# Performance work log

Measured on AMD Instinct MI355X. Metric: run time of the kernel, lower is better.

The kernel has to match this reference:

```python
import jax, jax.numpy as jnp
import numpy as np

B, N, D = 8, 1024, 768
H = 12
HD = D // H
LN_EPS = 1e-5
EPS = 1e-8


def setup_inputs() -> dict:
    key = jax.random.key(0)
    ks = jax.random.split(key, 16)
    s = 0.02
    return {
        "x": jax.random.normal(ks[0], (B, N, D), jnp.float32),
        "low_freq_feat": jax.random.normal(ks[1], (B, N, D), jnp.float32),
        "high_freq_feat": jax.random.normal(ks[2], (B, N, D), jnp.float32),
        "W_qkv_id": jax.random.normal(ks[3], (D, 3 * D), jnp.float32) * s,
        "W_qkv_attr": jax.random.normal(ks[4], (D, 3 * D), jnp.float32) * s,
        "W_fg_id": jax.random.normal(ks[5], (D, D), jnp.float32) * s,
        "b_fg_id": jnp.zeros((D,), jnp.float32),
        "W_fg_attr": jax.random.normal(ks[6], (D, D), jnp.float32) * s,
        "b_fg_attr": jnp.zeros((D,), jnp.float32),
        "W_proj_id": jax.random.normal(ks[7], (D, D), jnp.float32) * s,
        "b_proj_id": jnp.zeros((D,), jnp.float32),
        "W_proj_attr": jax.random.normal(ks[8], (D, D), jnp.float32) * s,
        "b_proj_attr": jnp.zeros((D,), jnp.float32),
        "ln_id_g": jnp.ones((D,), jnp.float32),
        "ln_id_b": jnp.zeros((D,), jnp.float32),
        "ln_attr_g": jnp.ones((D,), jnp.float32),
        "ln_attr_b": jnp.zeros((D,), jnp.float32),
        "ortho_temperature": jnp.float32(1.0),
        "freq_guide_strength": jnp.float32(0.3),
    }


def _layernorm(x, g, b):
    mu = x.mean(-1, keepdims=True)
    var = ((x - mu) ** 2).mean(-1, keepdims=True)
    return (x - mu) * jax.lax.rsqrt(var + LN_EPS) * g + b


def reference(x, low_freq_feat, high_freq_feat,
              W_qkv_id, W_qkv_attr,
              W_fg_id, b_fg_id, W_fg_attr, b_fg_attr,
              W_proj_id, b_proj_id, W_proj_attr, b_proj_attr,
              ln_id_g, ln_id_b, ln_attr_g, ln_attr_b,
              ortho_temperature, freq_guide_strength):
    b, n, d = x.shape
    scale = HD ** -0.5

    def split_qkv(t):
        t = t.reshape(b, n, 3, H, HD).transpose(2, 0, 3, 1, 4)
        return t[0], t[1], t[2]

    q_id, k_id, v_id = split_qkv(x @ W_qkv_id)
    q_at, k_at, v_at = split_qkv(x @ W_qkv_attr)

    fs = jax.nn.sigmoid(freq_guide_strength)
    low_g = (low_freq_feat @ W_fg_id + b_fg_id).reshape(b, n, H, HD).transpose(0, 2, 1, 3)
    high_g = (high_freq_feat @ W_fg_attr + b_fg_attr).reshape(b, n, H, HD).transpose(0, 2, 1, 3)
    v_id = v_id + fs * low_g
    v_at = v_at + fs * high_g

    def soft_attn(q, k):
        a = jnp.clip(jnp.einsum('bhnd,bhmd->bhnm', q, k) * scale, -20.0, 20.0)
        return jax.nn.softmax(a, axis=-1)

    attn_id = soft_attn(q_id, k_id)
    attn_at = soft_attn(q_at, k_at)

    # soft orthogonal mask (same mask for both branches)
    overlap = ((attn_id + EPS) * (attn_at + EPS)).sum(-1, keepdims=True)
    temp = jnp.clip(ortho_temperature, 0.1, 5.0)
    mask = jax.nn.sigmoid(-overlap * temp)

    def mask_renorm(a):
        m = a * mask
        m = m / (m.sum(-1, keepdims=True) + EPS)
        return jnp.where(jnp.isnan(m), jnp.zeros_like(m), m)

    attn_id = mask_renorm(attn_id)
    attn_at = mask_renorm(attn_at)

    def branch_out(a, v, W, bias, g, beta):
        o = jnp.einsum('bhnm,bhmd->bhnd', a, v).transpose(0, 2, 1, 3).reshape(b, n, d)
        return _layernorm(o @ W + bias, g, beta)

    id_features = branch_out(attn_id, v_id, W_proj_id, b_proj_id, ln_id_g, ln_id_b)
    attr_features = branch_out(attn_at, v_at, W_proj_attr, b_proj_attr, ln_attr_g, ln_attr_b)
    return (id_features, attr_features)
```

## Files before the change

kernel.cpp:

```cpp
#include <hip/hip_runtime.h>
#include <stdint.h>


typedef __attribute__((ext_vector_type(8))) _Float16 f16x8;
typedef __attribute__((ext_vector_type(4))) _Float16 f16x4;
typedef __attribute__((ext_vector_type(4))) float    f32x4;

__device__ __forceinline__ void g2l16(const void* g, void* l) {
  __builtin_amdgcn_global_load_lds(
      (const __attribute__((address_space(1))) void*)g,
      (__attribute__((address_space(3))) void*)l, 16, 0, 0);
}

template <bool SWAP>
__device__ __forceinline__ void gemm128(const _Float16* __restrict__ A,
                                        const _Float16* __restrict__ Bt,
                                        int K, int m0, int n0,
                                        _Float16* As, _Float16* Bs, f32x4* acc) {
  const int tid = threadIdx.x;
  const int lane = tid & 63, w = tid >> 6;
  const int wm = (w >> 1) * 64, wn = (w & 1) * 64;
  const int l15 = lane & 15, quad = lane >> 4;
  const int srow = lane >> 2;
  const int scol = ((lane & 3) ^ ((lane >> 3) & 3)) * 8;
  const int rg = (quad ^ ((l15 >> 1) & 3)) * 8;

#pragma unroll
  for (int i = 0; i < 16; i++) acc[i] = (f32x4){0.f, 0.f, 0.f, 0.f};

  const int KB = K >> 6;
#pragma unroll
  for (int k2 = 0; k2 < 2; k2++)
#pragma unroll
    for (int i = 0; i < 2; i++) {
      int c = w * 2 + i, row = c * 16 + srow;
      g2l16(A  + (size_t)(m0 + row) * K + k2 * 32 + scol, As + k2 * 4096 + c * 512);
      g2l16(Bt + (size_t)(n0 + row) * K + k2 * 32 + scol, Bs + k2 * 4096 + c * 512);
    }
  for (int kb = 0; kb < KB; kb++) {
    __syncthreads();
#pragma unroll
    for (int k2 = 0; k2 < 2; k2++) {
      f16x8 a[4], b[4];
#pragma unroll
      for (int mt = 0; mt < 4; mt++)
        a[mt] = *(const f16x8*)(As + k2 * 4096 + (wm + mt * 16 + l15) * 32 + rg);
#pragma unroll
      for (int nt = 0; nt < 4; nt++)
        b[nt] = *(const f16x8*)(Bs + k2 * 4096 + (wn + nt * 16 + l15) * 32 + rg);
#pragma unroll
      for (int mt = 0; mt < 4; mt++)
#pragma unroll
        for (int nt = 0; nt < 4; nt++)
          acc[mt * 4 + nt] = SWAP
              ? __builtin_amdgcn_mfma_f32_16x16x32_f16(b[nt], a[mt], acc[mt * 4 + nt], 0, 0, 0)
              : __builtin_amdgcn_mfma_f32_16x16x32_f16(a[mt], b[nt], acc[mt * 4 + nt], 0, 0, 0);
    }
    __syncthreads();
    if (kb + 1 < KB) {
      int k0 = (kb + 1) * 64;
#pragma unroll
      for (int k2 = 0; k2 < 2; k2++)
#pragma unroll
        for (int i = 0; i < 2; i++) {
          int c = w * 2 + i, row = c * 16 + srow;
          g2l16(A  + (size_t)(m0 + row) * K + k0 + k2 * 32 + scol, As + k2 * 4096 + c * 512);
          g2l16(Bt + (size_t)(n0 + row) * K + k0 + k2 * 32 + scol, Bs + k2 * 4096 + c * 512);
        }
    }
  }
}

__global__ __launch_bounds__(256) void k_cast3(const float* __restrict__ s0,
                                               const float* __restrict__ s1,
                                               const float* __restrict__ s2,
                                               _Float16* __restrict__ d0,
                                               _Float16* __restrict__ d1,
                                               _Float16* __restrict__ d2) {
  int blk = blockIdx.x;
  const float* s; _Float16* d;
  if (blk < 6144)       { s = s0; d = d0; }
  else if (blk < 12288) { s = s1; d = d1; blk -= 6144; }
  else                  { s = s2; d = d2; blk -= 12288; }
  int i = blk * 256 + threadIdx.x;
  float4 v = ((const float4*)s)[i];
  f16x4 o = {(_Float16)v.x, (_Float16)v.y, (_Float16)v.z, (_Float16)v.w};
  *(f16x4*)(d + (size_t)i * 4) = o;
}

__device__ __forceinline__ void tcast32(const float* __restrict__ src,
                                        _Float16* __restrict__ dst,
                                        int N, int n0, int k0) {
  __shared__ float t[32][33];
  int tr = threadIdx.x >> 5, tc = threadIdx.x & 31;
#pragma unroll
  for (int i = 0; i < 4; i++) {
    int r = tr + i * 8;
    t[r][tc] = src[(size_t)(k0 + r) * N + n0 + tc];
  }
  __syncthreads();
#pragma unroll
  for (int i = 0; i < 4; i++) {
    int r = tr + i * 8;
    dst[(size_t)(n0 + r) * 768 + k0 + tc] = (_Float16)t[tc][r];
  }
}

__global__ __launch_bounds__(256) void k_tcast_all(const float* __restrict__ Wq0,
                                                   const float* __restrict__ Wq1,
                                                   const float* __restrict__ W0,
                                                   const float* __restrict__ W1,
                                                   const float* __restrict__ W2,
                                                   const float* __restrict__ W3,
                                                   _Float16* __restrict__ Dq,
                                                   _Float16* __restrict__ D0,
                                                   _Float16* __restrict__ D1,
                                                   _Float16* __restrict__ D2,
                                                   _Float16* __restrict__ D3) {
  int blk = blockIdx.x;
  if (blk < 3456) {
    int half = blk / 1728, rem = blk % 1728;
    int xx = rem % 72, yy = rem / 72;
    tcast32(half ? Wq1 : Wq0, Dq + (size_t)half * 2304 * 768, 2304, xx * 32, yy * 32);
  } else {
    blk -= 3456;
    int q = blk / 576, rem = blk % 576;
    int xx = rem % 24, yy = rem / 24;
    const float* src; _Float16* d;
    if (q == 0)      { src = W0; d = D0; }
    else if (q == 1) { src = W1; d = D1; }
    else if (q == 2) { src = W2; d = D2; }
    else             { src = W3; d = D3; }
    tcast32(src, d, 768, xx * 32, yy * 32);
  }
}

__global__ __launch_bounds__(256) void k_gemm_qkv(const _Float16* __restrict__ A,
                                                  const _Float16* __restrict__ Bt,
                                                  _Float16* __restrict__ Qb,
                                                  _Float16* __restrict__ Kb,
                                                  _Float16* __restrict__ Vtb) {
  __shared__ alignas(16) _Float16 As[8192], Bs[8192];
  f32x4 acc[16];
  int m0 = blockIdx.y * 128, n0 = blockIdx.x * 128;
  int br = n0 / 2304;
  int three = (n0 - br * 2304) / 768;
  int lane = threadIdx.x & 63, w = threadIdx.x >> 6;
  int wm = (w >> 1) * 64, wn = (w & 1) * 64, l15 = lane & 15, quad = lane >> 4;

  if (three == 2) {
    gemm128<false>(A, Bt, 768, m0, n0, As, Bs, acc);
#pragma unroll
    for (int mt = 0; mt < 4; mt++)
#pragma unroll
      for (int nt = 0; nt < 4; nt++) {
        int n = n0 + wn + nt * 16 + l15;
        int c = n - br * 2304 - 1536;
        int h = c >> 6, hd = c & 63;
        int m = m0 + wm + mt * 16 + quad * 4;
        int b = m >> 10, tok = m & 1023;
        size_t head = (size_t)(br * 96 + b * 12 + h);
        f32x4 v = acc[mt * 4 + nt];
        f16x4 o;
#pragma unroll
        for (int r = 0; r < 4; r++) o[r] = (_Float16)v[r];
        *(f16x4*)(Vtb + (head * 64 + hd) * 1024 + tok) = o;
      }
  } else {
    gemm128<true>(A, Bt, 768, m0, n0, As, Bs, acc);
    float qscl = (three == 0) ? 0.125f * 1.44269504f : 1.0f;
    _Float16* dst = (three == 0) ? Qb : Kb;
#pragma unroll
    for (int mt = 0; mt < 4; mt++)
#pragma unroll
      for (int nt = 0; nt < 4; nt++) {
        int m = m0 + wm + mt * 16 + l15;
        int n = n0 + wn + nt * 16 + quad * 4;
        int c = n - br * 2304 - three * 768;
        int h = c >> 6, hd = c & 63;
        int b = m >> 10, tok = m & 1023;
        size_t head = (size_t)(br * 96 + b * 12 + h);
        f32x4 v = acc[mt * 4 + nt];
        f16x4 o;
#pragma unroll
        for (int r = 0; r < 4; r++) o[r] = (_Float16)(v[r] * qscl);
        *(f16x4*)(dst + (head * 1024 + tok) * 64 + hd) = o;
      }
  }
}

__global__ __launch_bounds__(256) void k_gemm_fgadd(const _Float16* __restrict__ Alo,
                                                    const _Float16* __restrict__ Ahi,
                                                    const _Float16* __restrict__ Bid,
                                                    const _Float16* __restrict__ Bat,
                                                    const float* __restrict__ bid,
                                                    const float* __restrict__ bat,
                                                    const float* __restrict__ fgs,
                                                    _Float16* __restrict__ Vtb) {
  __shared__ alignas(16) _Float16 As[8192], Bs[8192];
  f32x4 acc[16];
  int br = blockIdx.x / 6;
  int n0 = (blockIdx.x % 6) * 128, m0 = blockIdx.y * 128;
  const _Float16* A = br ? Ahi : Alo;
  const _Float16* Bt = br ? Bat : Bid;
  const float* bias = br ? bat : bid;
  gemm128<false>(A, Bt, 768, m0, n0, As, Bs, acc);
  float fs = 1.f / (1.f + __expf(-fgs[0]));
  int lane = threadIdx.x & 63, w = threadIdx.x >> 6;
  int wm = (w >> 1) * 64, wn = (w & 1) * 64, l15 = lane & 15, quad = lane >> 4;
#pragma unroll
  for (int mt = 0; mt < 4; mt++)
#pragma unroll
    for (int nt = 0; nt < 4; nt++) {
      int c = n0 + wn + nt * 16 + l15;
      int h = c >> 6, hd = c & 63;
      int m = m0 + wm + mt * 16 + quad * 4;
      int b = m >> 10, tok = m & 1023;
      size_t head = (size_t)(br * 96 + b * 12 + h);
      float bv = bias[c];
      f32x4 v = acc[mt * 4 + nt];
      _Float16* p = Vtb + (head * 64 + hd) * 1024 + tok;
      f16x4 old = *(const f16x4*)p;
      f16x4 o;
#pragma unroll
      for (int r = 0; r < 4; r++)
        o[r] = (_Float16)((float)old[r] + fs * (v[r] + bv));
      *(f16x4*)p = o;
    }
}

__global__ __launch_bounds__(256, 3) void k_attn(const _Float16* __restrict__ Qb,
                                                 const _Float16* __restrict__ Kb,
                                                 const _Float16* __restrict__ Vtb,
                                                 _Float16* __restrict__ Ob) {
  __shared__ alignas(16) _Float16 Qs[128 * 64];
  __shared__ alignas(16) _Float16 Ks[128 * 64];
  __shared__ alignas(16) _Float16 Vts[64 * 128];
  int hl = blockIdx.x;
  int br = hl / 96, bh = hl % 96;
  int qbase = blockIdx.y * 128;
  const _Float16* Qh = Qb + (size_t)hl * 65536;
  const _Float16* Kh = Kb + (size_t)hl * 65536;
  const _Float16* Vth = Vtb + (size_t)hl * 65536;
  int lane = threadIdx.x & 63, w = threadIdx.x >> 6;
  int l15 = lane & 15, quad = lane >> 4;
  const int key7 = l15 & 7;

  {
    int rr = lane >> 3, sg = (lane & 7) ^ rr;
#pragma unroll
    for (int i = 0; i < 4; i++) {
      int c = w * 4 + i;
      g2l16(Qh + (size_t)(qbase + c * 8 + rr) * 64 + sg * 8, Qs + c * 512);
    }
  }
  auto stage_kv = [&](int n0) {
    int rr8 = lane >> 3, sg8 = ((lane & 7) ^ rr8) * 8;
    int rr16 = lane >> 4;
#pragma unroll
    for (int i = 0; i < 4; i++) {
      int c = w * 4 + i;
      g2l16(Kh + (size_t)(n0 + c * 8 + rr8) * 64 + sg8, Ks + c * 512);
      int vrow = c * 4 + rr16;
      int sg16 = ((lane & 15) ^ (vrow & 15)) * 8;
      g2l16(Vth + (size_t)vrow * 1024 + n0 + sg16, Vts + c * 512);
    }
  };
  stage_kv(0);

  f32x4 o[2][4];
#pragma unroll
  for (int qg = 0; qg < 2; qg++)
#pragma unroll
    for (int i = 0; i < 4; i++) o[qg][i] = (f32x4){0.f, 0.f, 0.f, 0.f};
  float rs0 = 0.f, rs1 = 0.f;
  f16x8 bq[2][2];
  const f32x4 zero = (f32x4){0.f, 0.f, 0.f, 0.f};
  const int g0 = (quad ^ key7) * 8, g1 = ((4 + quad) ^ key7) * 8;

  for (int kt = 0; kt < 8; kt++) {
    __syncthreads();
    if (kt == 0) {
#pragma unroll
      for (int qg = 0; qg < 2; qg++) {
        bq[qg][0] = *(const f16x8*)(Qs + (w * 32 + qg * 16 + l15) * 64 + g0);
        bq[qg][1] = *(const f16x8*)(Qs + (w * 32 + qg * 16 + l15) * 64 + g1);
      }
    }
    f32x4 c0, c1;
    {
      f16x8 a0 = *(const f16x8*)(Ks + l15 * 64 + g0);
      f16x8 a1 = *(const f16x8*)(Ks + l15 * 64 + g1);
      c0 = __builtin_amdgcn_mfma_f32_16x16x32_f16(a0, bq[0][0], zero, 0, 0, 0);
      c0 = __builtin_amdgcn_mfma_f32_16x16x32_f16(a1, bq[0][1], c0, 0, 0, 0);
      c1 = __builtin_amdgcn_mfma_f32_16x16x32_f16(a0, bq[1][0], zero, 0, 0, 0);
      c1 = __builtin_amdgcn_mfma_f32_16x16x32_f16(a1, bq[1][1], c1, 0, 0, 0);
    }
#pragma unroll
    for (int nt = 0; nt < 8; nt++) {
      f32x4 n0_, n1_;
      if (nt < 7) {
        f16x8 a0 = *(const f16x8*)(Ks + ((nt + 1) * 16 + l15) * 64 + g0);
        f16x8 a1 = *(const f16x8*)(Ks + ((nt + 1) * 16 + l15) * 64 + g1);
        n0_ = __builtin_amdgcn_mfma_f32_16x16x32_f16(a0, bq[0][0], zero, 0, 0, 0);
        n0_ = __builtin_amdgcn_mfma_f32_16x16x32_f16(a1, bq[0][1], n0_, 0, 0, 0);
        n1_ = __builtin_amdgcn_mfma_f32_16x16x32_f16(a0, bq[1][0], zero, 0, 0, 0);
        n1_ = __builtin_amdgcn_mfma_f32_16x16x32_f16(a1, bq[1][1], n1_, 0, 0, 0);
      }
      f16x4 pt0, pt1;
#pragma unroll
      for (int r = 0; r < 4; r++) {
        float p = __builtin_amdgcn_exp2f(c0[r]);
        rs0 += p; pt0[r] = (_Float16)p;
      }
#pragma unroll
      for (int r = 0; r < 4; r++) {
        float p = __builtin_amdgcn_exp2f(c1[r]);
        rs1 += p; pt1[r] = (_Float16)p;
      }
#pragma unroll
      for (int hdt = 0; hdt < 4; hdt++) {
        int g = ((2 * nt + (quad >> 1)) ^ l15) * 8 + (quad & 1) * 4;
        f16x4 av = *(const f16x4*)(Vts + (hdt * 16 + l15) * 128 + g);
        o[0][hdt] = __builtin_amdgcn_mfma_f32_16x16x16f16(av, pt0, o[0][hdt], 0, 0, 0);
        o[1][hdt] = __builtin_amdgcn_mfma_f32_16x16x16f16(av, pt1, o[1][hdt], 0, 0, 0);
      }
      if (nt < 7) { c0 = n0_; c1 = n1_; }
    }
    __syncthreads();
    if (kt < 7) stage_kv((kt + 1) * 128);
  }
  int b = bh / 12, h = bh % 12;
#pragma unroll
  for (int qg = 0; qg < 2; qg++) {
    float l = qg ? rs1 : rs0;
    l += __shfl_xor(l, 16);
    l += __shfl_xor(l, 32);
    float inv = 1.f / l;
    size_t rowb = ((size_t)br * 8192 + b * 1024 + qbase + w * 32 + qg * 16 + l15) * 768 +
                  h * 64;
#pragma unroll
    for (int hdt = 0; hdt < 4; hdt++) {
      f16x4 u;
#pragma unroll
      for (int r = 0; r < 4; r++) u[r] = (_Float16)(o[qg][hdt][r] * inv);
      *(f16x4*)(Ob + rowb + hdt * 16 + quad * 4) = u;
    }
  }
}

__global__ __launch_bounds__(256) void k_gemm_proj2(const _Float16* __restrict__ Aid,
                                                    const _Float16* __restrict__ Aat,
                                                    const _Float16* __restrict__ Bid,
                                                    const _Float16* __restrict__ Bat,
                                                    _Float16* __restrict__ Yid,
                                                    _Float16* __restrict__ Yat) {
  __shared__ alignas(16) _Float16 As[8192], Bs[8192];
  f32x4 acc[16];
  int half = blockIdx.x / 6;
  int n0 = (blockIdx.x % 6) * 128, m0 = blockIdx.y * 128;
  const _Float16* A = half ? Aat : Aid;
  const _Float16* Bt = half ? Bat : Bid;
  _Float16* Y = half ? Yat : Yid;
  gemm128<true>(A, Bt, 768, m0, n0, As, Bs, acc);
  int lane = threadIdx.x & 63, w = threadIdx.x >> 6;
  int wm = (w >> 1) * 64, wn = (w & 1) * 64, l15 = lane & 15, quad = lane >> 4;
#pragma unroll
  for (int mt = 0; mt < 4; mt++)
#pragma unroll
    for (int nt = 0; nt < 4; nt++) {
      int m = m0 + wm + mt * 16 + l15;
      int n = n0 + wn + nt * 16 + quad * 4;
      f32x4 v = acc[mt * 4 + nt];
      f16x4 o;
#pragma unroll
      for (int r = 0; r < 4; r++) o[r] = (_Float16)v[r];
      *(f16x4*)(Y + (size_t)m * 768 + n) = o;
    }
}

__global__ __launch_bounds__(256) void k_ln(const _Float16* __restrict__ Yid,
                                            const _Float16* __restrict__ Yat,
                                            const float* __restrict__ bp_id,
                                            const float* __restrict__ bp_at,
                                            const float* __restrict__ g_id,
                                            const float* __restrict__ be_id,
                                            const float* __restrict__ g_at,
                                            const float* __restrict__ be_at,
                                            float* __restrict__ out) {
  int w = threadIdx.x >> 6, lane = threadIdx.x & 63;
  int r = blockIdx.x * 4 + w;
  int br = r >> 13, m = r & 8191;
  const _Float16* Y = br ? Yat : Yid;
  const float* bp = br ? bp_at : bp_id;
  const float* g = br ? g_at : g_id;
  const float* be = br ? be_at : be_id;
  float v[12], sum = 0.f, sq = 0.f;
#pragma unroll
  for (int j = 0; j < 3; j++) {
    int c = j * 256 + lane * 4;
    f16x4 y = *(const f16x4*)(Y + (size_t)m * 768 + c);
    float4 bv = *(const float4*)(bp + c);
#pragma unroll
    for (int r2 = 0; r2 < 4; r2++) {
      float t = (float)y[r2] + ((const float*)&bv)[r2];
      v[j * 4 + r2] = t; sum += t; sq += t * t;
    }
  }
#pragma unroll
  for (int d = 1; d < 64; d <<= 1) { sum += __shfl_xor(sum, d); sq += __shfl_xor(sq, d); }
  float mu = sum * (1.f / 768.f);
  float var = sq * (1.f / 768.f) - mu * mu;
  float rstd = rsqrtf(var + 1e-5f);
  float* op = out + (size_t)br * 6291456 + (size_t)m * 768;
#pragma unroll
  for (int j = 0; j < 3; j++) {
    int c = j * 256 + lane * 4;
    float4 gv = *(const float4*)(g + c);
    float4 bev = *(const float4*)(be + c);
    float4 ov;
#pragma unroll
    for (int r2 = 0; r2 < 4; r2++)
      ((float*)&ov)[r2] = (v[j * 4 + r2] - mu) * rstd * ((const float*)&gv)[r2] +
                          ((const float*)&bev)[r2];
    *(float4*)(op + c) = ov;
  }
}

extern "C" void kernel_launch(void* const* d_in, const int* in_sizes, int n_in,
                              void* d_out, int out_size, void* d_ws, size_t ws_size,
                              hipStream_t stream) {
  const float* x       = (const float*)d_in[0];
  const float* lowf    = (const float*)d_in[1];
  const float* highf   = (const float*)d_in[2];
  const float* Wqkv_id = (const float*)d_in[3];
  const float* Wqkv_at = (const float*)d_in[4];
  const float* Wfg_id  = (const float*)d_in[5];
  const float* bfg_id  = (const float*)d_in[6];
  const float* Wfg_at  = (const float*)d_in[7];
  const float* bfg_at  = (const float*)d_in[8];
  const float* Wpr_id  = (const float*)d_in[9];
  const float* bpr_id  = (const float*)d_in[10];
  const float* Wpr_at  = (const float*)d_in[11];
  const float* bpr_at  = (const float*)d_in[12];
  const float* g_id    = (const float*)d_in[13];
  const float* be_id   = (const float*)d_in[14];
  const float* g_at    = (const float*)d_in[15];
  const float* be_at   = (const float*)d_in[16];
  const float* fgs     = (const float*)d_in[18];

  char* ws = (char*)d_ws;
  _Float16* x_f    = (_Float16*)(ws + 0);
  _Float16* low_f  = (_Float16*)(ws + 12582912);
  _Float16* high_f = (_Float16*)(ws + 25165824);
  _Float16* wqkvt  = (_Float16*)(ws + 37748736);
  _Float16* wfgidt = (_Float16*)(ws + 44826624);
  _Float16* wfgatt = (_Float16*)(ws + 46006272);
  _Float16* wpridt = (_Float16*)(ws + 47185920);
  _Float16* wpratt = (_Float16*)(ws + 48365568);
  _Float16* Qb     = (_Float16*)(ws + 74711040);
  _Float16* Kb     = (_Float16*)(ws + 99876864);
  _Float16* Vtb    = (_Float16*)(ws + 125042688);
  _Float16* Ob     = (_Float16*)(ws + 150208512);
  _Float16* Y_id   = (_Float16*)(ws + 0);
  _Float16* Y_at   = (_Float16*)(ws + 49545216);

  k_cast3<<<18432, 256, 0, stream>>>(x, lowf, highf, x_f, low_f, high_f);
  k_tcast_all<<<5760, 256, 0, stream>>>(Wqkv_id, Wqkv_at, Wfg_id, Wfg_at, Wpr_id, Wpr_at,
                                        wqkvt, wfgidt, wfgatt, wpridt, wpratt);
  k_gemm_qkv<<<dim3(36, 64), 256, 0, stream>>>(x_f, wqkvt, Qb, Kb, Vtb);
  k_gemm_fgadd<<<dim3(12, 64), 256, 0, stream>>>(low_f, high_f, wfgidt, wfgatt,
                                                 bfg_id, bfg_at, fgs, Vtb);
  k_attn<<<dim3(192, 8), 256, 0, stream>>>(Qb, Kb, Vtb, Ob);
  k_gemm_proj2<<<dim3(12, 64), 256, 0, stream>>>(Ob, Ob + 6291456, wpridt, wpratt,
                                                 Y_id, Y_at);
  k_ln<<<4096, 256, 0, stream>>>(Y_id, Y_at, bpr_id, bpr_at, g_id, be_id, g_at, be_at,
                                 (float*)d_out);
}
```

Measured before the change: 423.0 us.

## Switch GEMMs to 256x256 tiles with 4-stage async LDS ring pipeline

Replaces the 128x128, 256-thread, double-sync GEMM core with a 256x256 tile computed by 512 threads (8 waves, each owning 128x64). It uses a 4-deep LDS ring buffer filled by global_load_lds, with explicit vmcnt waits and raw s_barriers, and splits A and B stage loads across two half-tiles. It also raises MFMA issue priority with s_setprio. The aim is more operand reuse per loaded byte and overlapping global-to-LDS transfers with MFMA work. The trade-off is 128KB of LDS per block, so likely one block per CU, and the fg and proj GEMMs now launch only 192 blocks, which risks underfilling the GPU and longer tails.

```diff
diff --git a/kernel.cpp b/kernel.cpp
--- a/kernel.cpp
+++ b/kernel.cpp
@@ -12,63 +12,102 @@
       (__attribute__((address_space(3))) void*)l, 16, 0, 0);
 }
 
+#define BARX()   asm volatile("s_barrier" ::: "memory")
+#define WAITV(N) asm volatile("s_waitcnt vmcnt(" #N ")" ::: "memory")
+
 template <bool SWAP>
-__device__ __forceinline__ void gemm128(const _Float16* __restrict__ A,
+__device__ __forceinline__ void gemm256(const _Float16* __restrict__ A,
                                         const _Float16* __restrict__ Bt,
                                         int K, int m0, int n0,
-                                        _Float16* As, _Float16* Bs, f32x4* acc) {
+                                        _Float16* As, _Float16* Bs,
+                                        f32x4 (&acc)[8][4]) {
   const int tid = threadIdx.x;
   const int lane = tid & 63, w = tid >> 6;
-  const int wm = (w >> 1) * 64, wn = (w & 1) * 64;
+  const int wm = (w >> 2) * 128, wn = (w & 3) * 64;
   const int l15 = lane & 15, quad = lane >> 4;
   const int srow = lane >> 2;
   const int scol = ((lane & 3) ^ ((lane >> 3) & 3)) * 8;
   const int rg = (quad ^ ((l15 >> 1) & 3)) * 8;
-
-#pragma unroll
-  for (int i = 0; i < 16; i++) acc[i] = (f32x4){0.f, 0.f, 0.f, 0.f};
-
-  const int KB = K >> 6;
-#pragma unroll
-  for (int k2 = 0; k2 < 2; k2++)
-#pragma unroll
-    for (int i = 0; i < 2; i++) {
-      int c = w * 2 + i, row = c * 16 + srow;
-      g2l16(A  + (size_t)(m0 + row) * K + k2 * 32 + scol, As + k2 * 4096 + c * 512);
-      g2l16(Bt + (size_t)(n0 + row) * K + k2 * 32 + scol, Bs + k2 * 4096 + c * 512);
-    }
-  for (int kb = 0; kb < KB; kb++) {
-    __syncthreads();
-#pragma unroll
-    for (int k2 = 0; k2 < 2; k2++) {
-      f16x8 a[4], b[4];
-#pragma unroll
-      for (int mt = 0; mt < 4; mt++)
-        a[mt] = *(const f16x8*)(As + k2 * 4096 + (wm + mt * 16 + l15) * 32 + rg);
-#pragma unroll
-      for (int nt = 0; nt < 4; nt++)
-        b[nt] = *(const f16x8*)(Bs + k2 * 4096 + (wn + nt * 16 + l15) * 32 + rg);
-#pragma unroll
-      for (int mt = 0; mt < 4; mt++)
-#pragma unroll
-        for (int nt = 0; nt < 4; nt++)
-          acc[mt * 4 + nt] = SWAP
-              ? __builtin_amdgcn_mfma_f32_16x16x32_f16(b[nt], a[mt], acc[mt * 4 + nt], 0, 0, 0)
-              : __builtin_amdgcn_mfma_f32_16x16x32_f16(a[mt], b[nt], acc[mt * 4 + nt], 0, 0, 0);
-    }
-    __syncthreads();
-    if (kb + 1 < KB) {
-      int k0 = (kb + 1) * 64;
-#pragma unroll
-      for (int k2 = 0; k2 < 2; k2++)
-#pragma unroll
-        for (int i = 0; i < 2; i++) {
-          int c = w * 2 + i, row = c * 16 + srow;
-          g2l16(A  + (size_t)(m0 + row) * K + k0 + k2 * 32 + scol, As + k2 * 4096 + c * 512);
-          g2l16(Bt + (size_t)(n0 + row) * K + k0 + k2 * 32 + scol, Bs + k2 * 4096 + c * 512);
-        }
-    }
-  }
+  const int c0 = w * 2, c1 = c0 + 1;
+  const _Float16* pA0 = A + (m0 + c0 * 16 + srow) * K + scol;
+  const _Float16* pA1 = A + (m0 + c1 * 16 + srow) * K + scol;
+  const _Float16* pB0 = Bt + (n0 + c0 * 16 + srow) * K + scol;
+  const _Float16* pB1 = Bt + (n0 + c1 * 16 + srow) * K + scol;
+
+#pragma unroll
+  for (int mt = 0; mt < 8; mt++)
+#pragma unroll
+    for (int nt = 0; nt < 4; nt++) acc[mt][nt] = (f32x4){0.f, 0.f, 0.f, 0.f};
+
+  const int KT = K >> 5;
+
+#pragma unroll
+  for (int t = 0; t < 3; t++) {
+    int kc = t * 32, bj = t * 8192;
+    g2l16(pA0 + kc, As + bj + c0 * 512);
+    g2l16(pB0 + kc, Bs + bj + c0 * 512);
+    g2l16(pA1 + kc, As + bj + c1 * 512);
+    g2l16(pB1 + kc, Bs + bj + c1 * 512);
+  }
+  WAITV(8);
+  BARX();
+
+  auto tile = [&](int t, bool doStage) {
+    const int bj = (t & 3) * 8192;
+    const _Float16* as = As + bj;
+    const _Float16* bs = Bs + bj;
+    const int kcn = (t + 3) * 32;
+    const int bn = ((t + 3) & 3) * 8192;
+    f16x8 a[8];
+#pragma unroll
+    for (int mt = 0; mt < 8; mt++)
+      a[mt] = *(const f16x8*)(as + (wm + mt * 16 + l15) * 32 + rg);
+    f16x8 b0 = *(const f16x8*)(bs + (wn + l15) * 32 + rg);
+    f16x8 b1 = *(const f16x8*)(bs + (wn + 16 + l15) * 32 + rg);
+    if (doStage) {
+      g2l16(pA0 + kcn, As + bn + c0 * 512);
+      g2l16(pA1 + kcn, As + bn + c1 * 512);
+    }
+    __builtin_amdgcn_s_setprio(1);
+#pragma unroll
+    for (int mt = 0; mt < 8; mt++) {
+      acc[mt][0] = SWAP
+          ? __builtin_amdgcn_mfma_f32_16x16x32_f16(b0, a[mt], acc[mt][0], 0, 0, 0)
+          : __builtin_amdgcn_mfma_f32_16x16x32_f16(a[mt], b0, acc[mt][0], 0, 0, 0);
+      acc[mt][1] = SWAP
+          ? __builtin_amdgcn_mfma_f32_16x16x32_f16(b1, a[mt], acc[mt][1], 0, 0, 0)
+          : __builtin_amdgcn_mfma_f32_16x16x32_f16(a[mt], b1, acc[mt][1], 0, 0, 0);
+    }
+    __builtin_amdgcn_s_setprio(0);
+    BARX();
+    f16x8 b2 = *(const f16x8*)(bs + (wn + 32 + l15) * 32 + rg);
+    f16x8 b3 = *(const f16x8*)(bs + (wn + 48 + l15) * 32 + rg);
+    if (doStage) {
+      g2l16(pB0 + kcn, Bs + bn + c0 * 512);
+      g2l16(pB1 + kcn, Bs + bn + c1 * 512);
+    }
+    __builtin_amdgcn_s_setprio(1);
+#pragma unroll
+    for (int mt = 0; mt < 8; mt++) {
+      acc[mt][2] = SWAP
+          ? __builtin_amdgcn_mfma_f32_16x16x32_f16(b2, a[mt], acc[mt][2], 0, 0, 0)
+          : __builtin_amdgcn_mfma_f32_16x16x32_f16(a[mt], b2, acc[mt][2], 0, 0, 0);
+      acc[mt][3] = SWAP
+          ? __builtin_amdgcn_mfma_f32_16x16x32_f16(b3, a[mt], acc[mt][3], 0, 0, 0)
+          : __builtin_amdgcn_mfma_f32_16x16x32_f16(a[mt], b3, acc[mt][3], 0, 0, 0);
+    }
+    __builtin_amdgcn_s_setprio(0);
+  };
+
+  int t = 0;
+  for (; t < KT - 3; ++t) {
+    tile(t, true);
+    WAITV(8);
+    BARX();
+  }
+  tile(t, false); WAITV(4); BARX(); ++t;
+  tile(t, false); WAITV(0); BARX(); ++t;
+  tile(t, false);
 }
 
 __global__ __launch_bounds__(256) void k_cast3(const float* __restrict__ s0,
@@ -135,23 +174,23 @@
   }
 }
 
-__global__ __launch_bounds__(256) void k_gemm_qkv(const _Float16* __restrict__ A,
-                                                  const _Float16* __restrict__ Bt,
-                                                  _Float16* __restrict__ Qb,
-                                                  _Float16* __restrict__ Kb,
-                                                  _Float16* __restrict__ Vtb) {
-  __shared__ alignas(16) _Float16 As[8192], Bs[8192];
-  f32x4 acc[16];
-  int m0 = blockIdx.y * 128, n0 = blockIdx.x * 128;
+__global__ __launch_bounds__(512, 2) void k_gemm_qkv(const _Float16* __restrict__ A,
+                                                     const _Float16* __restrict__ Bt,
+                                                     _Float16* __restrict__ Qb,
+                                                     _Float16* __restrict__ Kb,
+                                                     _Float16* __restrict__ Vtb) {
+  __shared__ alignas(16) _Float16 As[32768], Bs[32768];
+  f32x4 acc[8][4];
+  int m0 = blockIdx.y * 256, n0 = blockIdx.x * 256;
   int br = n0 / 2304;
   int three = (n0 - br * 2304) / 768;
   int lane = threadIdx.x & 63, w = threadIdx.x >> 6;
-  int wm = (w >> 1) * 64, wn = (w & 1) * 64, l15 = lane & 15, quad = lane >> 4;
+  int wm = (w >> 2) * 128, wn = (w & 3) * 64, l15 = lane & 15, quad = lane >> 4;
 
   if (three == 2) {
-    gemm128<false>(A, Bt, 768, m0, n0, As, Bs, acc);
-#pragma unroll
-    for (int mt = 0; mt < 4; mt++)
+    gemm256<false>(A, Bt, 768, m0, n0, As, Bs, acc);
+#pragma unroll
+    for (int mt = 0; mt < 8; mt++)
 #pragma unroll
       for (int nt = 0; nt < 4; nt++) {
         int n = n0 + wn + nt * 16 + l15;
@@ -160,18 +199,18 @@
         int m = m0 + wm + mt * 16 + quad * 4;
         int b = m >> 10, tok = m & 1023;
         size_t head = (size_t)(br * 96 + b * 12 + h);
-        f32x4 v = acc[mt * 4 + nt];
+        f32x4 v = acc[mt][nt];
         f16x4 o;
 #pragma unroll
         for (int r = 0; r < 4; r++) o[r] = (_Float16)v[r];
         *(f16x4*)(Vtb + (head * 64 + hd) * 1024 + tok) = o;
       }
   } else {
-    gemm128<true>(A, Bt, 768, m0, n0, As, Bs, acc);
+    gemm256<true>(A, Bt, 768, m0, n0, As, Bs, acc);
     float qscl = (three == 0) ? 0.125f * 1.44269504f : 1.0f;
     _Float16* dst = (three == 0) ? Qb : Kb;
 #pragma unroll
-    for (int mt = 0; mt < 4; mt++)
+    for (int mt = 0; mt < 8; mt++)
 #pragma unroll
       for (int nt = 0; nt < 4; nt++) {
         int m = m0 + wm + mt * 16 + l15;
@@ -180,7 +219,7 @@
         int h = c >> 6, hd = c & 63;
         int b = m >> 10, tok = m & 1023;
         size_t head = (size_t)(br * 96 + b * 12 + h);
-        f32x4 v = acc[mt * 4 + nt];
+        f32x4 v = acc[mt][nt];
         f16x4 o;
 #pragma unroll
         for (int r = 0; r < 4; r++) o[r] = (_Float16)(v[r] * qscl);
@@ -189,27 +228,27 @@
   }
 }
 
-__global__ __launch_bounds__(256) void k_gemm_fgadd(const _Float16* __restrict__ Alo,
-                                                    const _Float16* __restrict__ Ahi,
-                                                    const _Float16* __restrict__ Bid,
-                                                    const _Float16* __restrict__ Bat,
-                                                    const float* __restrict__ bid,
-                                                    const float* __restrict__ bat,
-                                                    const float* __restrict__ fgs,
-                                                    _Float16* __restrict__ Vtb) {
-  __shared__ alignas(16) _Float16 As[8192], Bs[8192];
-  f32x4 acc[16];
-  int br = blockIdx.x / 6;
-  int n0 = (blockIdx.x % 6) * 128, m0 = blockIdx.y * 128;
+__global__ __launch_bounds__(512, 2) void k_gemm_fgadd(const _Float16* __restrict__ Alo,
+                                                       const _Float16* __restrict__ Ahi,
+                                                       const _Float16* __restrict__ Bid,
+                                                       const _Float16* __restrict__ Bat,
+                                                       const float* __restrict__ bid,
+                                                       const float* __restrict__ bat,
+                                                       const float* __restrict__ fgs,
+                                                       _Float16* __restrict__ Vtb) {
+  __shared__ alignas(16) _Float16 As[32768], Bs[32768];
+  f32x4 acc[8][4];
+  int br = blockIdx.x / 3;
+  int n0 = (blockIdx.x % 3) * 256, m0 = blockIdx.y * 256;
   const _Float16* A = br ? Ahi : Alo;
   const _Float16* Bt = br ? Bat : Bid;
   const float* bias = br ? bat : bid;
-  gemm128<false>(A, Bt, 768, m0, n0, As, Bs, acc);
+  gemm256<false>(A, Bt, 768, m0, n0, As, Bs, acc);
   float fs = 1.f / (1.f + __expf(-fgs[0]));
   int lane = threadIdx.x & 63, w = threadIdx.x >> 6;
-  int wm = (w >> 1) * 64, wn = (w & 1) * 64, l15 = lane & 15, quad = lane >> 4;
-#pragma unroll
-  for (int mt = 0; mt < 4; mt++)
+  int wm = (w >> 2) * 128, wn = (w & 3) * 64, l15 = lane & 15, quad = lane >> 4;
+#pragma unroll
+  for (int mt = 0; mt < 8; mt++)
 #pragma unroll
     for (int nt = 0; nt < 4; nt++) {
       int c = n0 + wn + nt * 16 + l15;
@@ -218,7 +257,7 @@
       int b = m >> 10, tok = m & 1023;
       size_t head = (size_t)(br * 96 + b * 12 + h);
       float bv = bias[c];
-      f32x4 v = acc[mt * 4 + nt];
+      f32x4 v = acc[mt][nt];
       _Float16* p = Vtb + (head * 64 + hd) * 1024 + tok;
       f16x4 old = *(const f16x4*)p;
       f16x4 o;
@@ -349,29 +388,29 @@
   }
 }
 
-__global__ __launch_bounds__(256) void k_gemm_proj2(const _Float16* __restrict__ Aid,
-                                                    const _Float16* __restrict__ Aat,
-                                                    const _Float16* __restrict__ Bid,
-                                                    const _Float16* __restrict__ Bat,
-                                                    _Float16* __restrict__ Yid,
-                                                    _Float16* __restrict__ Yat) {
-  __shared__ alignas(16) _Float16 As[8192], Bs[8192];
-  f32x4 acc[16];
-  int half = blockIdx.x / 6;
-  int n0 = (blockIdx.x % 6) * 128, m0 = blockIdx.y * 128;
+__global__ __launch_bounds__(512, 2) void k_gemm_proj2(const _Float16* __restrict__ Aid,
+                                                       const _Float16* __restrict__ Aat,
+                                                       const _Float16* __restrict__ Bid,
+                                                       const _Float16* __restrict__ Bat,
+                                                       _Float16* __restrict__ Yid,
+                                                       _Float16* __restrict__ Yat) {
+  __shared__ alignas(16) _Float16 As[32768], Bs[32768];
+  f32x4 acc[8][4];
+  int half = blockIdx.x / 3;
+  int n0 = (blockIdx.x % 3) * 256, m0 = blockIdx.y * 256;
   const _Float16* A = half ? Aat : Aid;
   const _Float16* Bt = half ? Bat : Bid;
   _Float16* Y = half ? Yat : Yid;
-  gemm128<true>(A, Bt, 768, m0, n0, As, Bs, acc);
+  gemm256<true>(A, Bt, 768, m0, n0, As, Bs, acc);
   int lane = threadIdx.x & 63, w = threadIdx.x >> 6;
-  int wm = (w >> 1) * 64, wn = (w & 1) * 64, l15 = lane & 15, quad = lane >> 4;
-#pragma unroll
-  for (int mt = 0; mt < 4; mt++)
+  int wm = (w >> 2) * 128, wn = (w & 3) * 64, l15 = lane & 15, quad = lane >> 4;
+#pragma unroll
+  for (int mt = 0; mt < 8; mt++)
 #pragma unroll
     for (int nt = 0; nt < 4; nt++) {
       int m = m0 + wm + mt * 16 + l15;
       int n = n0 + wn + nt * 16 + quad * 4;
-      f32x4 v = acc[mt * 4 + nt];
+      f32x4 v = acc[mt][nt];
       f16x4 o;
 #pragma unroll
       for (int r = 0; r < 4; r++) o[r] = (_Float16)v[r];
@@ -468,12 +507,12 @@
   k_cast3<<<18432, 256, 0, stream>>>(x, lowf, highf, x_f, low_f, high_f);
   k_tcast_all<<<5760, 256, 0, stream>>>(Wqkv_id, Wqkv_at, Wfg_id, Wfg_at, Wpr_id, Wpr_at,
                                         wqkvt, wfgidt, wfgatt, wpridt, wpratt);
-  k_gemm_qkv<<<dim3(36, 64), 256, 0, stream>>>(x_f, wqkvt, Qb, Kb, Vtb);
-  k_gemm_fgadd<<<dim3(12, 64), 256, 0, stream>>>(low_f, high_f, wfgidt, wfgatt,
-                                                 bfg_id, bfg_at, fgs, Vtb);
+  k_gemm_qkv<<<dim3(18, 32), 512, 0, stream>>>(x_f, wqkvt, Qb, Kb, Vtb);
+  k_gemm_fgadd<<<dim3(6, 32), 512, 0, stream>>>(low_f, high_f, wfgidt, wfgatt,
+                                                bfg_id, bfg_at, fgs, Vtb);
   k_attn<<<dim3(192, 8), 256, 0, stream>>>(Qb, Kb, Vtb, Ob);
-  k_gemm_proj2<<<dim3(12, 64), 256, 0, stream>>>(Ob, Ob + 6291456, wpridt, wpratt,
-                                                 Y_id, Y_at);
+  k_gemm_proj2<<<dim3(6, 32), 512, 0, stream>>>(Ob, Ob + 6291456, wpridt, wpratt,
+                                                Y_id, Y_at);
   k_ln<<<4096, 256, 0, stream>>>(Y_id, Y_at, bpr_id, bpr_at, g_id, be_id, g_at, be_at,
                                  (float*)d_out);
 }
```

New measurement: 410.3 us. -3.0%, faster.

## Enlarge GEMM tiles to 256x192 with double-buffered LDS and MFMA priority

Applied to the files above, without the earlier changes.

The shared GEMM helper now uses 256x192 block tiles with 512 threads, each wave computing 64x96. LDS is double-buffered so the next K-tile's global-to-LDS loads are issued before the current tile's MFMAs, replacing two __syncthreads per iteration with one vmcnt wait and barrier. The MFMA section also raises wave priority and is fenced with scheduling barriers. The goal is more operand reuse per LDS load, fewer barriers and load latency hidden behind compute. In exchange it uses more LDS and more registers per block, and launches far fewer blocks, which may leave CUs unevenly loaded.

```diff
diff --git a/kernel.cpp b/kernel.cpp
--- a/kernel.cpp
+++ b/kernel.cpp
@@ -12,62 +12,81 @@
       (__attribute__((address_space(3))) void*)l, 16, 0, 0);
 }
 
+#define BARX()   asm volatile("s_barrier" ::: "memory")
+#define WAITV0() asm volatile("s_waitcnt vmcnt(0)" ::: "memory")
+
 template <bool SWAP>
-__device__ __forceinline__ void gemm128(const _Float16* __restrict__ A,
+__device__ __forceinline__ void gemm192(const _Float16* __restrict__ A,
                                         const _Float16* __restrict__ Bt,
                                         int K, int m0, int n0,
-                                        _Float16* As, _Float16* Bs, f32x4* acc) {
+                                        _Float16* As, _Float16* Bs,
+                                        f32x4 (&acc)[4][6]) {
   const int tid = threadIdx.x;
   const int lane = tid & 63, w = tid >> 6;
-  const int wm = (w >> 1) * 64, wn = (w & 1) * 64;
+  const int wm = (w >> 1) * 64, wn = (w & 1) * 96;
   const int l15 = lane & 15, quad = lane >> 4;
   const int srow = lane >> 2;
   const int scol = ((lane & 3) ^ ((lane >> 3) & 3)) * 8;
   const int rg = (quad ^ ((l15 >> 1) & 3)) * 8;
-
-#pragma unroll
-  for (int i = 0; i < 16; i++) acc[i] = (f32x4){0.f, 0.f, 0.f, 0.f};
-
-  const int KB = K >> 6;
-#pragma unroll
-  for (int k2 = 0; k2 < 2; k2++)
-#pragma unroll
-    for (int i = 0; i < 2; i++) {
-      int c = w * 2 + i, row = c * 16 + srow;
-      g2l16(A  + (size_t)(m0 + row) * K + k2 * 32 + scol, As + k2 * 4096 + c * 512);
-      g2l16(Bt + (size_t)(n0 + row) * K + k2 * 32 + scol, Bs + k2 * 4096 + c * 512);
-    }
-  for (int kb = 0; kb < KB; kb++) {
-    __syncthreads();
-#pragma unroll
-    for (int k2 = 0; k2 < 2; k2++) {
-      f16x8 a[4], b[4];
+  const int KT = K >> 6;
+
+  auto stage = [&](int t) {
+    const int kc = t * 64;
+    _Float16* Ab = As + (t & 1) * 16384;
+    _Float16* Bb = Bs + (t & 1) * 12288;
+#pragma unroll
+    for (int h = 0; h < 2; h++)
+#pragma unroll
+      for (int i = 0; i < 2; i++) {
+        int c = w * 2 + i;
+        g2l16(A + (size_t)(m0 + c * 16 + srow) * K + kc + h * 32 + scol,
+              Ab + h * 8192 + c * 512);
+      }
+#pragma unroll
+    for (int i = 0; i < 3; i++) {
+      int j = w * 3 + i;
+      int hb = j / 12, cb = j % 12;
+      g2l16(Bt + (size_t)(n0 + cb * 16 + srow) * K + kc + hb * 32 + scol,
+            Bb + hb * 6144 + cb * 512);
+    }
+  };
+
+#pragma unroll
+  for (int mt = 0; mt < 4; mt++)
+#pragma unroll
+    for (int nt = 0; nt < 6; nt++) acc[mt][nt] = (f32x4){0.f, 0.f, 0.f, 0.f};
+
+  stage(0);
+  WAITV0();
+  BARX();
+
+  for (int t = 0; t < KT; t++) {
+    const _Float16* as = As + (t & 1) * 16384;
+    const _Float16* bs = Bs + (t & 1) * 12288;
+    if (t + 1 < KT) stage(t + 1);
+#pragma unroll
+    for (int ks = 0; ks < 2; ks++) {
+      f16x8 a[4], b[6];
 #pragma unroll
       for (int mt = 0; mt < 4; mt++)
-        a[mt] = *(const f16x8*)(As + k2 * 4096 + (wm + mt * 16 + l15) * 32 + rg);
-#pragma unroll
-      for (int nt = 0; nt < 4; nt++)
-        b[nt] = *(const f16x8*)(Bs + k2 * 4096 + (wn + nt * 16 + l15) * 32 + rg);
+        a[mt] = *(const f16x8*)(as + ks * 8192 + (wm + mt * 16 + l15) * 32 + rg);
+#pragma unroll
+      for (int nt = 0; nt < 6; nt++)
+        b[nt] = *(const f16x8*)(bs + ks * 6144 + (wn + nt * 16 + l15) * 32 + rg);
+      __builtin_amdgcn_sched_barrier(0);
+      __builtin_amdgcn_s_setprio(1);
 #pragma unroll
       for (int mt = 0; mt < 4; mt++)
 #pragma unroll
-        for (int nt = 0; nt < 4; nt++)
-          acc[mt * 4 + nt] = SWAP
-              ? __builtin_amdgcn_mfma_f32_16x16x32_f16(b[nt], a[mt], acc[mt * 4 + nt], 0, 0, 0)
-              : __builtin_amdgcn_mfma_f32_16x16x32_f16(a[mt], b[nt], acc[mt * 4 + nt], 0, 0, 0);
-    }
-    __syncthreads();
-    if (kb + 1 < KB) {
-      int k0 = (kb + 1) * 64;
-#pragma unroll
-      for (int k2 = 0; k2 < 2; k2++)
-#pragma unroll
-        for (int i = 0; i < 2; i++) {
-          int c = w * 2 + i, row = c * 16 + srow;
-          g2l16(A  + (size_t)(m0 + row) * K + k0 + k2 * 32 + scol, As + k2 * 4096 + c * 512);
-          g2l16(Bt + (size_t)(n0 + row) * K + k0 + k2 * 32 + scol, Bs + k2 * 4096 + c * 512);
-        }
-    }
+        for (int nt = 0; nt < 6; nt++)
+          acc[mt][nt] = SWAP
+              ? __builtin_amdgcn_mfma_f32_16x16x32_f16(b[nt], a[mt], acc[mt][nt], 0, 0, 0)
+              : __builtin_amdgcn_mfma_f32_16x16x32_f16(a[mt], b[nt], acc[mt][nt], 0, 0, 0);
+      __builtin_amdgcn_s_setprio(0);
+      __builtin_amdgcn_sched_barrier(0);
+    }
+    WAITV0();
+    BARX();
   }
 }
 
@@ -135,52 +154,52 @@
   }
 }
 
-__global__ __launch_bounds__(256) void k_gemm_qkv(const _Float16* __restrict__ A,
-                                                  const _Float16* __restrict__ Bt,
-                                                  _Float16* __restrict__ Qb,
-                                                  _Float16* __restrict__ Kb,
-                                                  _Float16* __restrict__ Vtb) {
-  __shared__ alignas(16) _Float16 As[8192], Bs[8192];
-  f32x4 acc[16];
-  int m0 = blockIdx.y * 128, n0 = blockIdx.x * 128;
+__global__ __launch_bounds__(512, 2) void k_gemm_qkv(const _Float16* __restrict__ A,
+                                                     const _Float16* __restrict__ Bt,
+                                                     _Float16* __restrict__ Qb,
+                                                     _Float16* __restrict__ Kb,
+                                                     _Float16* __restrict__ Vtb) {
+  __shared__ alignas(16) _Float16 As[32768], Bs[24576];
+  f32x4 acc[4][6];
+  int m0 = blockIdx.y * 256, n0 = blockIdx.x * 192;
   int br = n0 / 2304;
   int three = (n0 - br * 2304) / 768;
   int lane = threadIdx.x & 63, w = threadIdx.x >> 6;
-  int wm = (w >> 1) * 64, wn = (w & 1) * 64, l15 = lane & 15, quad = lane >> 4;
+  int wm = (w >> 1) * 64, wn = (w & 1) * 96, l15 = lane & 15, quad = lane >> 4;
 
   if (three == 2) {
-    gemm128<false>(A, Bt, 768, m0, n0, As, Bs, acc);
+    gemm192<false>(A, Bt, 768, m0, n0, As, Bs, acc);
 #pragma unroll
     for (int mt = 0; mt < 4; mt++)
 #pragma unroll
-      for (int nt = 0; nt < 4; nt++) {
+      for (int nt = 0; nt < 6; nt++) {
         int n = n0 + wn + nt * 16 + l15;
         int c = n - br * 2304 - 1536;
         int h = c >> 6, hd = c & 63;
         int m = m0 + wm + mt * 16 + quad * 4;
         int b = m >> 10, tok = m & 1023;
         size_t head = (size_t)(br * 96 + b * 12 + h);
-        f32x4 v = acc[mt * 4 + nt];
+        f32x4 v = acc[mt][nt];
         f16x4 o;
 #pragma unroll
         for (int r = 0; r < 4; r++) o[r] = (_Float16)v[r];
         *(f16x4*)(Vtb + (head * 64 + hd) * 1024 + tok) = o;
       }
   } else {
-    gemm128<true>(A, Bt, 768, m0, n0, As, Bs, acc);
+    gemm192<true>(A, Bt, 768, m0, n0, As, Bs, acc);
     float qscl = (three == 0) ? 0.125f * 1.44269504f : 1.0f;
     _Float16* dst = (three == 0) ? Qb : Kb;
 #pragma unroll
     for (int mt = 0; mt < 4; mt++)
 #pragma unroll
-      for (int nt = 0; nt < 4; nt++) {
+      for (int nt = 0; nt < 6; nt++) {
         int m = m0 + wm + mt * 16 + l15;
         int n = n0 + wn + nt * 16 + quad * 4;
         int c = n - br * 2304 - three * 768;
         int h = c >> 6, hd = c & 63;
         int b = m >> 10, tok = m & 1023;
         size_t head = (size_t)(br * 96 + b * 12 + h);
-        f32x4 v = acc[mt * 4 + nt];
+        f32x4 v = acc[mt][nt];
         f16x4 o;
 #pragma unroll
         for (int r = 0; r < 4; r++) o[r] = (_Float16)(v[r] * qscl);
@@ -189,36 +208,36 @@
   }
 }
 
-__global__ __launch_bounds__(256) void k_gemm_fgadd(const _Float16* __restrict__ Alo,
-                                                    const _Float16* __restrict__ Ahi,
-                                                    const _Float16* __restrict__ Bid,
-                                                    const _Float16* __restrict__ Bat,
-                                                    const float* __restrict__ bid,
-                                                    const float* __restrict__ bat,
-                                                    const float* __restrict__ fgs,
-                                                    _Float16* __restrict__ Vtb) {
-  __shared__ alignas(16) _Float16 As[8192], Bs[8192];
-  f32x4 acc[16];
-  int br = blockIdx.x / 6;
-  int n0 = (blockIdx.x % 6) * 128, m0 = blockIdx.y * 128;
+__global__ __launch_bounds__(512, 2) void k_gemm_fgadd(const _Float16* __restrict__ Alo,
+                                                       const _Float16* __restrict__ Ahi,
+                                                       const _Float16* __restrict__ Bid,
+                                                       const _Float16* __restrict__ Bat,
+                                                       const float* __restrict__ bid,
+                                                       const float* __restrict__ bat,
+                                                       const float* __restrict__ fgs,
+                                                       _Float16* __restrict__ Vtb) {
+  __shared__ alignas(16) _Float16 As[32768], Bs[24576];
+  f32x4 acc[4][6];
+  int br = blockIdx.x >> 2;
+  int n0 = (blockIdx.x & 3) * 192, m0 = blockIdx.y * 256;
   const _Float16* A = br ? Ahi : Alo;
   const _Float16* Bt = br ? Bat : Bid;
   const float* bias = br ? bat : bid;
-  gemm128<false>(A, Bt, 768, m0, n0, As, Bs, acc);
+  gemm192<false>(A, Bt, 768, m0, n0, As, Bs, acc);
   float fs = 1.f / (1.f + __expf(-fgs[0]));
   int lane = threadIdx.x & 63, w = threadIdx.x >> 6;
-  int wm = (w >> 1) * 64, wn = (w & 1) * 64, l15 = lane & 15, quad = lane >> 4;
+  int wm = (w >> 1) * 64, wn = (w & 1) * 96, l15 = lane & 15, quad = lane >> 4;
 #pragma unroll
   for (int mt = 0; mt < 4; mt++)
 #pragma unroll
-    for (int nt = 0; nt < 4; nt++) {
+    for (int nt = 0; nt < 6; nt++) {
       int c = n0 + wn + nt * 16 + l15;
       int h = c >> 6, hd = c & 63;
       int m = m0 + wm + mt * 16 + quad * 4;
       int b = m >> 10, tok = m & 1023;
       size_t head = (size_t)(br * 96 + b * 12 + h);
       float bv = bias[c];
-      f32x4 v = acc[mt * 4 + nt];
+      f32x4 v = acc[mt][nt];
       _Float16* p = Vtb + (head * 64 + hd) * 1024 + tok;
       f16x4 old = *(const f16x4*)p;
       f16x4 o;
@@ -349,29 +368,29 @@
   }
 }
 
-__global__ __launch_bounds__(256) void k_gemm_proj2(const _Float16* __restrict__ Aid,
-                                                    const _Float16* __restrict__ Aat,
-                                                    const _Float16* __restrict__ Bid,
-                                                    const _Float16* __restrict__ Bat,
-                                                    _Float16* __restrict__ Yid,
-                                                    _Float16* __restrict__ Yat) {
-  __shared__ alignas(16) _Float16 As[8192], Bs[8192];
-  f32x4 acc[16];
-  int half = blockIdx.x / 6;
-  int n0 = (blockIdx.x % 6) * 128, m0 = blockIdx.y * 128;
+__global__ __launch_bounds__(512, 2) void k_gemm_proj2(const _Float16* __restrict__ Aid,
+                                                       const _Float16* __restrict__ Aat,
+                                                       const _Float16* __restrict__ Bid,
+                                                       const _Float16* __restrict__ Bat,
+                                                       _Float16* __restrict__ Yid,
+                                                       _Float16* __restrict__ Yat) {
+  __shared__ alignas(16) _Float16 As[32768], Bs[24576];
+  f32x4 acc[4][6];
+  int half = blockIdx.x >> 2;
+  int n0 = (blockIdx.x & 3) * 192, m0 = blockIdx.y * 256;
   const _Float16* A = half ? Aat : Aid;
   const _Float16* Bt = half ? Bat : Bid;
   _Float16* Y = half ? Yat : Yid;
-  gemm128<true>(A, Bt, 768, m0, n0, As, Bs, acc);
+  gemm192<true>(A, Bt, 768, m0, n0, As, Bs, acc);
   int lane = threadIdx.x & 63, w = threadIdx.x >> 6;
-  int wm = (w >> 1) * 64, wn = (w & 1) * 64, l15 = lane & 15, quad = lane >> 4;
+  int wm = (w >> 1) * 64, wn = (w & 1) * 96, l15 = lane & 15, quad = lane >> 4;
 #pragma unroll
   for (int mt = 0; mt < 4; mt++)
 #pragma unroll
-    for (int nt = 0; nt < 4; nt++) {
+    for (int nt = 0; nt < 6; nt++) {
       int m = m0 + wm + mt * 16 + l15;
       int n = n0 + wn + nt * 16 + quad * 4;
-      f32x4 v = acc[mt * 4 + nt];
+      f32x4 v = acc[mt][nt];
       f16x4 o;
 #pragma unroll
       for (int r = 0; r < 4; r++) o[r] = (_Float16)v[r];
@@ -468,12 +487,12 @@
   k_cast3<<<18432, 256, 0, stream>>>(x, lowf, highf, x_f, low_f, high_f);
   k_tcast_all<<<5760, 256, 0, stream>>>(Wqkv_id, Wqkv_at, Wfg_id, Wfg_at, Wpr_id, Wpr_at,
                                         wqkvt, wfgidt, wfgatt, wpridt, wpratt);
-  k_gemm_qkv<<<dim3(36, 64), 256, 0, stream>>>(x_f, wqkvt, Qb, Kb, Vtb);
-  k_gemm_fgadd<<<dim3(12, 64), 256, 0, stream>>>(low_f, high_f, wfgidt, wfgatt,
-                                                 bfg_id, bfg_at, fgs, Vtb);
+  k_gemm_qkv<<<dim3(24, 32), 512, 0, stream>>>(x_f, wqkvt, Qb, Kb, Vtb);
+  k_gemm_fgadd<<<dim3(8, 32), 512, 0, stream>>>(low_f, high_f, wfgidt, wfgatt,
+                                                bfg_id, bfg_at, fgs, Vtb);
   k_attn<<<dim3(192, 8), 256, 0, stream>>>(Qb, Kb, Vtb, Ob);
-  k_gemm_proj2<<<dim3(12, 64), 256, 0, stream>>>(Ob, Ob + 6291456, wpridt, wpratt,
-                                                 Y_id, Y_at);
+  k_gemm_proj2<<<dim3(8, 32), 512, 0, stream>>>(Ob, Ob + 6291456, wpridt, wpratt,
+                                                Y_id, Y_at);
   k_ln<<<4096, 256, 0, stream>>>(Y_id, Y_at, bpr_id, bpr_at, g_id, be_id, g_at, be_at,
                                  (float*)d_out);
 }
```

After: 434.3 us. 1.03x slower.
